# Kernel optimization log

Measured on AMD Instinct MI355X. Metric: run time of the kernel, lower is better.

Reference implementation:

```python
import jax, jax.numpy as jnp
import numpy as np

IC, IND, MID, OC, OD, ITERS = 8, 16, 32, 8, 16, 3
B, H, W = 8, 64, 64


def squash(x, axis):
    sq = jnp.sum(x * x, axis=axis, keepdims=True)
    return sq / (0.5 + sq) * x / (jnp.sqrt(sq + 1e-6) + 1e-6)


def gconv(x, w, b, pad):
    # grouped conv over the IC capsule groups (equivalent to the per-capsule
    # Conv2d blocks applied to slices of the capsule axis)
    y = jax.lax.conv_general_dilated(
        x, w, (1, 1), pad,
        dimension_numbers=("NCHW", "OIHW", "NCHW"),
        feature_group_count=IC)
    return y + b[None, :, None, None]


def setup_inputs() -> dict:
    key = jax.random.key(0)
    ks = jax.random.split(key, 7)
    x = jax.random.normal(ks[0], (B, IC * IND, H, W), jnp.float32)
    w1 = jax.random.normal(ks[1], (IC * MID, IND, 1, 1), jnp.float32) * 0.1
    b1 = jax.random.normal(ks[2], (IC * MID,), jnp.float32) * 0.1
    w2 = jax.random.normal(ks[3], (IC * MID, MID, 3, 3), jnp.float32) * 0.05
    b2 = jax.random.normal(ks[4], (IC * MID,), jnp.float32) * 0.1
    w3 = jax.random.normal(ks[5], (IC * OC * OD, MID, 1, 1), jnp.float32) * 0.05
    b3 = jax.random.normal(ks[6], (IC * OC * OD,), jnp.float32) * 0.1
    attn_w = jnp.zeros((1, OC, 1, 1, 1), jnp.float32)  # torch init: zeros
    attn_b = jnp.ones((1, OC, 1, 1, 1), jnp.float32)   # torch init: ones
    return dict(x=x, w1=w1, b1=b1, w2=w2, b2=b2, w3=w3, b3=b3,
                attn_w=attn_w, attn_b=attn_b)


def reference(x, w1, b1, w2, b2, w3, b3, attn_w, attn_b):
    bsz = x.shape[0]
    h_, w_ = x.shape[-2], x.shape[-1]
    # per-capsule conv stack: ReLU -> 1x1 -> ReLU -> 3x3 -> ReLU -> 1x1
    h = jax.nn.relu(x)
    h = jax.nn.relu(gconv(h, w1, b1, "VALID"))
    h = jax.nn.relu(gconv(h, w2, b2, "SAME"))
    h = gconv(h, w3, b3, "VALID")                     # [B, IC*OC*OD, H, W]
    u_hat = h.reshape(bsz, IC, OC, OD, h_, w_)
    u_sq = squash(u_hat, axis=3)
    # dynamic routing
    b = jnp.zeros((bsz, IC, OC, h_, w_), u_hat.dtype)
    for _ in range(ITERS - 1):
        c = jax.nn.sigmoid(b)
        s = jnp.sum(u_sq * c[:, :, :, None], axis=1)   # [B, OC, OD, H, W]
        v = squash(s, axis=2)
        b = b + jnp.sum(u_sq * v[:, None], axis=3)     # [B, IC, OC, H, W]
    c = jax.nn.sigmoid(b)
    s = jnp.sum(u_hat * c[:, :, :, None], axis=1)      # [B, OC, OD, H, W]
    # SpatialCapsuleAttn
    mean_hw = jnp.mean(s, axis=(-2, -1), keepdims=True)        # adaptive avg pool(1)
    avg = jnp.sum(s * mean_hw, axis=2)                         # [B, OC, H, W]
    t = avg.reshape(bsz, OC, h_ * w_)
    m = jnp.mean(t, axis=-1, keepdims=True)
    sd = jnp.std(t, axis=-1, keepdims=True, ddof=1) + 1e-6     # torch std: unbiased
    t = (t - m) / sd
    t = t.reshape(bsz, OC, 1, h_, w_) * attn_w + attn_b
    s = s * jax.nn.sigmoid(t)
    out = s.reshape(bsz, OC * OD, h_, w_) + x
    return out
```

## Files before the change

### kernel.cpp

```cpp
#include <hip/hip_runtime.h>
#include <hip/hip_bf16.h>
#include <hip/hip_fp16.h>

#define HW 4096

typedef _Float16 f16x8 __attribute__((ext_vector_type(8)));
typedef float f32x4 __attribute__((ext_vector_type(4)));

#define FOR8(X) X(0) X(1) X(2) X(3) X(4) X(5) X(6) X(7)

static __device__ __forceinline__ __half2 u2h(unsigned int u) {
    union { unsigned int u; __half2 h; } c; c.u = u; return c.h;
}
static __device__ __forceinline__ unsigned int h2u(__half2 h) {
    union { unsigned int u; __half2 h; } c; c.h = h; return c.u;
}

__global__ __launch_bounds__(256) void k0_prep(const float* __restrict__ w3, ushort* __restrict__ w3h,
                                               const float* __restrict__ w2, ushort* __restrict__ w2f) {
    int bid = blockIdx.x;
    int t = threadIdx.x;
    if (bid < 128) {
        int gi = bid * 256 + t;
        int j = gi & 7;
        int l = (gi >> 3) & 63;
        int p = gi >> 9;
        int ic = p >> 3, oc = p & 7;
        int od = l & 15;
        int m  = ((l >> 4) << 3) + j;
        w3h[gi] = __half_as_ushort(__float2half(w3[(size_t)((ic * 128 + oc * 16 + od) * 32 + m)]));
    } else {
        int gi = (bid - 128) * 256 + t;
        if (gi >= 73728) return;
        int j   = gi & 7;
        int l   = (gi >> 3) & 63;
        int h   = (gi >> 9) & 1;
        int tap = (gi >> 10) % 9;
        int g   = gi / 9216;
        int co = h * 16 + (l & 15);
        int ci = ((l >> 4) << 3) + j;
        w2f[gi] = __half_as_ushort(__float2half(w2[(size_t)((g * 32 + co) * 32 + ci) * 9 + tap]));
    }
}

__global__ __launch_bounds__(256) void k12_conv(const float* __restrict__ x, const float* __restrict__ w1,
                                                const float* __restrict__ b1, const ushort* __restrict__ w2f,
                                                const float* __restrict__ b2, ushort* __restrict__ h2g) {
    __shared__ ushort h1s[3][66][40];

    int bi = blockIdx.x;
    int y  = bi & 63;
    int g  = (bi >> 6) & 7;
    int b  = bi >> 9;
    int t  = threadIdx.x;

    if (t < 198) {
        int r  = t / 66;
        int xi = t - r * 66;
        int yy = y + r - 1;
        int xx = xi - 1;
        bool valid = (yy >= 0) && (yy < 64) && (xx >= 0) && (xx < 64);
        ushort hv[32];
        if (valid) {
            const float* xb = x + (size_t)(b * 128 + g * 16) * HW + yy * 64 + xx;
            float xv[16];
#pragma unroll
            for (int i = 0; i < 16; ++i) xv[i] = fmaxf(xb[i * HW], 0.f);
            const float* wg = w1 + g * 512;
            const float* bg = b1 + g * 32;
#pragma unroll
            for (int m = 0; m < 32; ++m) {
                float acc = bg[m];
#pragma unroll
                for (int i = 0; i < 16; ++i) acc = fmaf(xv[i], wg[m * 16 + i], acc);
                hv[m] = __half_as_ushort(__float2half(fmaxf(acc, 0.f)));
            }
        } else {
#pragma unroll
            for (int m = 0; m < 32; ++m) hv[m] = 0;
        }
        ushort* dst = &h1s[r][xi][0];
#pragma unroll
        for (int q = 0; q < 4; ++q) *(uint4*)&dst[q * 8] = *(uint4*)&hv[q * 8];
    }
    __syncthreads();

    int w  = t >> 6, l = t & 63;
    int lrow = l & 15, kgrp = l >> 4;
    int xcol = w * 16 + lrow;

    f16x8 Bf[9];
#pragma unroll
    for (int dy = 0; dy < 3; ++dy)
#pragma unroll
        for (int dx = 0; dx < 3; ++dx)
            Bf[dy * 3 + dx] = *(const f16x8*)&h1s[dy][xcol + dx][kgrp * 8];

    const ushort* wg2 = w2f + (size_t)g * 9216;
    f16x8 Af[9][2];
#pragma unroll
    for (int tap = 0; tap < 9; ++tap)
#pragma unroll
        for (int h = 0; h < 2; ++h)
            Af[tap][h] = *(const f16x8*)&wg2[((tap * 2 + h) * 64 + l) * 8];

    f32x4 acc[2];
#pragma unroll
    for (int h = 0; h < 2; ++h) {
        float4 bias = *(const float4*)(b2 + g * 32 + h * 16 + kgrp * 4);
        acc[h][0] = bias.x; acc[h][1] = bias.y; acc[h][2] = bias.z; acc[h][3] = bias.w;
    }
#pragma unroll
    for (int tap = 0; tap < 9; ++tap) {
#pragma unroll
        for (int h = 0; h < 2; ++h)
            acc[h] = __builtin_amdgcn_mfma_f32_16x16x32_f16(Af[tap][h], Bf[tap], acc[h], 0, 0, 0);
    }

    int px = y * 64 + xcol;
    ushort* ob = h2g + ((size_t)(b * 8 + g) * HW + px) * 32;
#pragma unroll
    for (int h = 0; h < 2; ++h) {
        __half2 lo = __floats2half2_rn(fmaxf(acc[h][0], 0.f), fmaxf(acc[h][1], 0.f));
        __half2 hi = __floats2half2_rn(fmaxf(acc[h][2], 0.f), fmaxf(acc[h][3], 0.f));
        uint2 wv; wv.x = h2u(lo); wv.y = h2u(hi);
        *(uint2*)&ob[h * 16 + kgrp * 4] = wv;
    }
}

__global__ __launch_bounds__(512) void k3f_route(const ushort* __restrict__ h2g, const ushort* __restrict__ w3h,
                                                 const float* __restrict__ b3, ushort* __restrict__ sOut,
                                                 float* __restrict__ part) {
    __shared__ ushort us[32 * 1024];
    __shared__ float wred[8][16][8];
    int bid = blockIdx.x;
    int b   = bid >> 7;
    int px0 = (bid & 127) << 5;
    int t   = threadIdx.x;
    int w   = t >> 6, l = t & 63;

    {
        int ic = w;
        int lrow = l & 15, lk = l >> 4;
        f16x8 bf0 = *(const f16x8*)&h2g[(((size_t)(b * 8 + ic)) * HW + px0 + lrow) * 32 + lk * 8];
        f16x8 bf1 = *(const f16x8*)&h2g[(((size_t)(b * 8 + ic)) * HW + px0 + 16 + lrow) * 32 + lk * 8];
        int s0sw = (lrow & 15) << 3;
#pragma unroll
        for (int oc = 0; oc < 8; ++oc) {
            f16x8 af = *(const f16x8*)&w3h[((ic * 8 + oc) * 64 + l) * 8];
            float4 bv = *(const float4*)(b3 + ic * 128 + oc * 16 + lk * 4);
            f32x4 c0; c0[0] = bv.x; c0[1] = bv.y; c0[2] = bv.z; c0[3] = bv.w;
            int ch = ic * 128 + oc * 16 + lk * 4;
            f32x4 d0 = __builtin_amdgcn_mfma_f32_16x16x32_f16(af, bf0, c0, 0, 0, 0);
            uint2 wv0;
            wv0.x = h2u(__floats2half2_rn(d0[0], d0[1]));
            wv0.y = h2u(__floats2half2_rn(d0[2], d0[3]));
            *(uint2*)&us[lrow * 1024 + (ch ^ s0sw)] = wv0;
            f32x4 d1 = __builtin_amdgcn_mfma_f32_16x16x32_f16(af, bf1, c0, 0, 0, 0);
            uint2 wv1;
            wv1.x = h2u(__floats2half2_rn(d1[0], d1[1]));
            wv1.y = h2u(__floats2half2_rn(d1[2], d1[3]));
            *(uint2*)&us[(16 + lrow) * 1024 + (ch ^ s0sw)] = wv1;
        }
    }
    __syncthreads();

    int px  = t >> 4;
    int oc  = (t >> 1) & 7;
    int odh = t & 1;
    int ssw = (px & 15) << 3;
    const ushort* ur = &us[px * 1024];
#define LDQ(i) uint4 q##i = *(const uint4*)&ur[((i) * 128 + oc * 16 + odh * 8) ^ ssw];
    FOR8(LDQ)
#undef LDQ
    __syncthreads();

#define UNP(i) float2 f0 = __half22float2(u2h(q##i.x)), f1 = __half22float2(u2h(q##i.y)), \
                      f2 = __half22float2(u2h(q##i.z)), f3 = __half22float2(u2h(q##i.w));

#define SC(i) float sc##i; { UNP(i) \
        float sp = f0.x*f0.x + f0.y*f0.y + f1.x*f1.x + f1.y*f1.y \
                 + f2.x*f2.x + f2.y*f2.y + f3.x*f3.x + f3.y*f3.y; \
        sp += __shfl_xor(sp, 1); \
        sc##i = sp / ((0.5f + sp) * (sqrtf(sp + 1e-6f) + 1e-6f)); }
    FOR8(SC)
#undef SC

#define BRI(i) float br##i = 0.f;
    FOR8(BRI)
#undef BRI

    float s0, s1, s2, s3, s4, s5, s6, s7;
#pragma unroll
    for (int it = 0; it < 2; ++it) {
#define CSC(i) float cs##i = sc##i / (1.f + __expf(-br##i));
        FOR8(CSC)
#undef CSC
        s0 = s1 = s2 = s3 = s4 = s5 = s6 = s7 = 0.f;
#define SVA(i) { UNP(i) \
        s0 = fmaf(f0.x, cs##i, s0); s1 = fmaf(f0.y, cs##i, s1); \
        s2 = fmaf(f1.x, cs##i, s2); s3 = fmaf(f1.y, cs##i, s3); \
        s4 = fmaf(f2.x, cs##i, s4); s5 = fmaf(f2.y, cs##i, s5); \
        s6 = fmaf(f3.x, cs##i, s6); s7 = fmaf(f3.y, cs##i, s7); }
        FOR8(SVA)
#undef SVA
        float sp = s0*s0 + s1*s1 + s2*s2 + s3*s3 + s4*s4 + s5*s5 + s6*s6 + s7*s7;
        sp += __shfl_xor(sp, 1);
        float f = sp / ((0.5f + sp) * (sqrtf(sp + 1e-6f) + 1e-6f));
#define DOTD(i) { UNP(i) \
        float dp = f0.x*s0 + f0.y*s1 + f1.x*s2 + f1.y*s3 + f2.x*s4 + f2.y*s5 + f3.x*s6 + f3.y*s7; \
        dp += __shfl_xor(dp, 1); \
        br##i = fmaf(sc##i * f, dp, br##i); }
        FOR8(DOTD)
#undef DOTD
    }

#define CF(i) float cf##i = 1.f / (1.f + __expf(-br##i));
    FOR8(CF)
#undef CF
    s0 = s1 = s2 = s3 = s4 = s5 = s6 = s7 = 0.f;
#define FS(i) { UNP(i) \
        s0 = fmaf(f0.x, cf##i, s0); s1 = fmaf(f0.y, cf##i, s1); \
        s2 = fmaf(f1.x, cf##i, s2); s3 = fmaf(f1.y, cf##i, s3); \
        s4 = fmaf(f2.x, cf##i, s4); s5 = fmaf(f2.y, cf##i, s5); \
        s6 = fmaf(f3.x, cf##i, s6); s7 = fmaf(f3.y, cf##i, s7); }
    FOR8(FS)
#undef FS
#undef UNP

    {
        uint4 pk;
        pk.x = h2u(__floats2half2_rn(s0, s1));
        pk.y = h2u(__floats2half2_rn(s2, s3));
        pk.z = h2u(__floats2half2_rn(s4, s5));
        pk.w = h2u(__floats2half2_rn(s6, s7));
        *(uint4*)&us[px * 1024 + ((oc * 16 + odh * 8) ^ ssw)] = pk;
    }

    {
        float p0 = s0, p1 = s1, p2 = s2, p3 = s3, p4 = s4, p5 = s5, p6 = s6, p7 = s7;
#pragma unroll
        for (int m = 16; m <= 32; m <<= 1) {
            p0 += __shfl_xor(p0, m); p1 += __shfl_xor(p1, m);
            p2 += __shfl_xor(p2, m); p3 += __shfl_xor(p3, m);
            p4 += __shfl_xor(p4, m); p5 += __shfl_xor(p5, m);
            p6 += __shfl_xor(p6, m); p7 += __shfl_xor(p7, m);
        }
        if ((l & 48) == 0) {
            float* wr = wred[w][oc * 2 + odh];
            wr[0] = p0; wr[1] = p1; wr[2] = p2; wr[3] = p3;
            wr[4] = p4; wr[5] = p5; wr[6] = p6; wr[7] = p7;
        }
    }
    __syncthreads();

    {
        int oc2 = w;
        int pxw = l >> 1, half = l & 1;
        int ch2 = (oc2 * 16 + half * 8) ^ ((pxw & 15) << 3);
        uint4 v = *(const uint4*)&us[pxw * 1024 + ch2];
        ushort* sb = sOut + ((size_t)(b * 8 + oc2) * 4096 + px0 + pxw) * 16 + half * 8;
        *(uint4*)sb = v;
    }
    if (t < 128) {
        int comb = t >> 3, j = t & 7;
        float a = 0.f;
#pragma unroll
        for (int ww = 0; ww < 8; ++ww) a += wred[ww][comb][j];
        int oc3 = comb >> 1, odh3 = comb & 1;
        part[((size_t)(b * 8 + oc3) * 128 + (bid & 127)) * 16 + odh3 * 8 + j] = a;
    }
}

__global__ __launch_bounds__(256) void k4_avg(const ushort* __restrict__ sIn, const float* __restrict__ part,
                                              float* __restrict__ avg, float* __restrict__ stats) {
    __shared__ float mh[16];
    int bi = blockIdx.x;
    int chunk = bi & 15;
    int bo = bi >> 4;
    int t = threadIdx.x;
    int pos = chunk * 256 + t;

    if (t < 16) {
        float a = 0.f;
        for (int c = 0; c < 128; ++c) a += part[(size_t)(bo * 128 + c) * 16 + t];
        mh[t] = a * (1.f / 4096.f);
    }
    __syncthreads();

    const ushort* sb = sIn + ((size_t)bo * 4096 + pos) * 16;
    uint4 qa = *(const uint4*)&sb[0];
    uint4 qb = *(const uint4*)&sb[8];
    float2 f0 = __half22float2(u2h(qa.x)), f1 = __half22float2(u2h(qa.y));
    float2 f2 = __half22float2(u2h(qa.z)), f3 = __half22float2(u2h(qa.w));
    float2 f4 = __half22float2(u2h(qb.x)), f5 = __half22float2(u2h(qb.y));
    float2 f6 = __half22float2(u2h(qb.z)), f7 = __half22float2(u2h(qb.w));
    float a = f0.x * mh[0] + f0.y * mh[1] + f1.x * mh[2] + f1.y * mh[3]
            + f2.x * mh[4] + f2.y * mh[5] + f3.x * mh[6] + f3.y * mh[7]
            + f4.x * mh[8] + f4.y * mh[9] + f5.x * mh[10] + f5.y * mh[11]
            + f6.x * mh[12] + f6.y * mh[13] + f7.x * mh[14] + f7.y * mh[15];
    avg[(size_t)bo * 4096 + pos] = a;

    float p1 = a, p2 = a * a;
#pragma unroll
    for (int m = 1; m < 64; m <<= 1) {
        p1 += __shfl_xor(p1, m);
        p2 += __shfl_xor(p2, m);
    }
    if ((t & 63) == 0) {
        atomicAdd(&stats[bo * 2],     p1);
        atomicAdd(&stats[bo * 2 + 1], p2);
    }
}

__global__ __launch_bounds__(256) void k5_out(const ushort* __restrict__ sIn, const float* __restrict__ x,
                                              const float* __restrict__ avg, const float* __restrict__ stats,
                                              const float* __restrict__ aw, const float* __restrict__ ab,
                                              float* __restrict__ out) {
    int bi = blockIdx.x;
    int chunk = bi & 15;
    int bo = bi >> 4;
    int oc = bo & 7;
    int pos = chunk * 256 + threadIdx.x;

    float sum = stats[bo * 2], sumsq = stats[bo * 2 + 1];
    float m   = sum * (1.f / 4096.f);
    float var = (sumsq - 4096.f * m * m) * (1.f / 4095.f);
    float sd  = sqrtf(fmaxf(var, 0.f)) + 1e-6f;

    float t   = (avg[(size_t)bo * 4096 + pos] - m) / sd * aw[oc] + ab[oc];
    float sig = 1.f / (1.f + __expf(-t));

    const ushort* sb = sIn + ((size_t)bo * 4096 + pos) * 16;
    uint4 qa = *(const uint4*)&sb[0];
    uint4 qb = *(const uint4*)&sb[8];
    float2 f0 = __half22float2(u2h(qa.x)), f1 = __half22float2(u2h(qa.y));
    float2 f2 = __half22float2(u2h(qa.z)), f3 = __half22float2(u2h(qa.w));
    float2 f4 = __half22float2(u2h(qb.x)), f5 = __half22float2(u2h(qb.y));
    float2 f6 = __half22float2(u2h(qb.z)), f7 = __half22float2(u2h(qb.w));
    float sv[16] = {f0.x, f0.y, f1.x, f1.y, f2.x, f2.y, f3.x, f3.y,
                    f4.x, f4.y, f5.x, f5.y, f6.x, f6.y, f7.x, f7.y};

    const float* xb = x + (size_t)bo * 16 * HW + pos;
    float* ob = out + (size_t)bo * 16 * HW + pos;
#pragma unroll
    for (int od = 0; od < 16; ++od) ob[od * HW] = fmaf(sv[od], sig, xb[od * HW]);
}

extern "C" void kernel_launch(void* const* d_in, const int* in_sizes, int n_in,
                              void* d_out, int out_size, void* d_ws, size_t ws_size,
                              hipStream_t stream) {
    const float* x  = (const float*)d_in[0];
    const float* w1 = (const float*)d_in[1];
    const float* b1 = (const float*)d_in[2];
    const float* w2 = (const float*)d_in[3];
    const float* b2 = (const float*)d_in[4];
    const float* w3 = (const float*)d_in[5];
    const float* b3 = (const float*)d_in[6];
    const float* aw = (const float*)d_in[7];
    const float* ab = (const float*)d_in[8];

    float* ws      = (float*)d_ws;
    ushort* h2g    = (ushort*)ws;
    ushort* sbuf   = (ushort*)(ws + 4194304);
    float* avg     = ws + 4194304 + 2097152;
    float* part    = avg + 262144;
    float* stats   = part + 131072;
    ushort* w3h    = (ushort*)(stats + 128);
    ushort* w2f    = w3h + 32768;

    hipMemsetAsync(stats, 0, 128 * sizeof(float), stream);
    k0_prep  <<<416, 256, 0, stream>>>(w3, w3h, w2, w2f);
    k12_conv <<<4096, 256, 0, stream>>>(x, w1, b1, w2f, b2, h2g);
    k3f_route<<<1024, 512, 0, stream>>>(h2g, w3h, b3, sbuf, part);
    k4_avg   <<<1024, 256, 0, stream>>>(sbuf, part, avg, stats);
    k5_out   <<<1024, 256, 0, stream>>>(sbuf, x, avg, stats, aw, ab, (float*)d_out);
}
```

Before: 94.33 us.

## Process four output rows per conv block to reuse halo rows; fold stats memset into prep

The fused 1x1+3x3 conv kernel now computes four output rows per block instead of one. It stages six input rows of the 1x1 output in shared memory rather than three, so halo recomputation drops from 3x to 1.5x, and the grid shrinks fourfold. Each wave loops over four 16-column tiles and loads its A and B fragments per tap inside the loop instead of preloading them. The separate hipMemsetAsync for the stats buffer is replaced by zeroing it in the prep kernel, which removes one launch. The trade-offs are fewer blocks in flight, lower parallelism, and repeated weight loads from global or L1 memory inside the tile loop.

```diff
diff --git a/kernel.cpp b/kernel.cpp
--- a/kernel.cpp
+++ b/kernel.cpp
@@ -17,9 +17,11 @@
 }
 
 __global__ __launch_bounds__(256) void k0_prep(const float* __restrict__ w3, ushort* __restrict__ w3h,
-                                               const float* __restrict__ w2, ushort* __restrict__ w2f) {
+                                               const float* __restrict__ w2, ushort* __restrict__ w2f,
+                                               float* __restrict__ stats) {
     int bid = blockIdx.x;
     int t = threadIdx.x;
+    if (bid == 0 && t < 128) stats[t] = 0.f;
     if (bid < 128) {
         int gi = bid * 256 + t;
         int j = gi & 7;
@@ -46,18 +48,19 @@
 __global__ __launch_bounds__(256) void k12_conv(const float* __restrict__ x, const float* __restrict__ w1,
                                                 const float* __restrict__ b1, const ushort* __restrict__ w2f,
                                                 const float* __restrict__ b2, ushort* __restrict__ h2g) {
-    __shared__ ushort h1s[3][66][40];
+    __shared__ ushort h1s[6][66][40];
 
     int bi = blockIdx.x;
-    int y  = bi & 63;
-    int g  = (bi >> 6) & 7;
-    int b  = bi >> 9;
+    int q  = bi & 15;
+    int g  = (bi >> 4) & 7;
+    int b  = bi >> 7;
+    int y0 = q * 4;
     int t  = threadIdx.x;
 
-    if (t < 198) {
-        int r  = t / 66;
-        int xi = t - r * 66;
-        int yy = y + r - 1;
+    for (int i = t; i < 396; i += 256) {
+        int r  = i / 66;
+        int xi = i - r * 66;
+        int yy = y0 + r - 1;
         int xx = xi - 1;
         bool valid = (yy >= 0) && (yy < 64) && (xx >= 0) && (xx < 64);
         ushort hv[32];
@@ -65,14 +68,14 @@
             const float* xb = x + (size_t)(b * 128 + g * 16) * HW + yy * 64 + xx;
             float xv[16];
 #pragma unroll
-            for (int i = 0; i < 16; ++i) xv[i] = fmaxf(xb[i * HW], 0.f);
+            for (int i2 = 0; i2 < 16; ++i2) xv[i2] = fmaxf(xb[i2 * HW], 0.f);
             const float* wg = w1 + g * 512;
             const float* bg = b1 + g * 32;
 #pragma unroll
             for (int m = 0; m < 32; ++m) {
                 float acc = bg[m];
 #pragma unroll
-                for (int i = 0; i < 16; ++i) acc = fmaf(xv[i], wg[m * 16 + i], acc);
+                for (int i2 = 0; i2 < 16; ++i2) acc = fmaf(xv[i2], wg[m * 16 + i2], acc);
                 hv[m] = __half_as_ushort(__float2half(fmaxf(acc, 0.f)));
             }
         } else {
@@ -81,50 +84,42 @@
         }
         ushort* dst = &h1s[r][xi][0];
 #pragma unroll
-        for (int q = 0; q < 4; ++q) *(uint4*)&dst[q * 8] = *(uint4*)&hv[q * 8];
+        for (int q2 = 0; q2 < 4; ++q2) *(uint4*)&dst[q2 * 8] = *(uint4*)&hv[q2 * 8];
     }
     __syncthreads();
 
     int w  = t >> 6, l = t & 63;
     int lrow = l & 15, kgrp = l >> 4;
-    int xcol = w * 16 + lrow;
-
-    f16x8 Bf[9];
-#pragma unroll
-    for (int dy = 0; dy < 3; ++dy)
-#pragma unroll
-        for (int dx = 0; dx < 3; ++dx)
-            Bf[dy * 3 + dx] = *(const f16x8*)&h1s[dy][xcol + dx][kgrp * 8];
-
+    int yloc = w;
     const ushort* wg2 = w2f + (size_t)g * 9216;
-    f16x8 Af[9][2];
-#pragma unroll
-    for (int tap = 0; tap < 9; ++tap)
-#pragma unroll
-        for (int h = 0; h < 2; ++h)
-            Af[tap][h] = *(const f16x8*)&wg2[((tap * 2 + h) * 64 + l) * 8];
-
-    f32x4 acc[2];
-#pragma unroll
-    for (int h = 0; h < 2; ++h) {
-        float4 bias = *(const float4*)(b2 + g * 32 + h * 16 + kgrp * 4);
-        acc[h][0] = bias.x; acc[h][1] = bias.y; acc[h][2] = bias.z; acc[h][3] = bias.w;
-    }
-#pragma unroll
-    for (int tap = 0; tap < 9; ++tap) {
-#pragma unroll
-        for (int h = 0; h < 2; ++h)
-            acc[h] = __builtin_amdgcn_mfma_f32_16x16x32_f16(Af[tap][h], Bf[tap], acc[h], 0, 0, 0);
-    }
-
-    int px = y * 64 + xcol;
-    ushort* ob = h2g + ((size_t)(b * 8 + g) * HW + px) * 32;
-#pragma unroll
-    for (int h = 0; h < 2; ++h) {
-        __half2 lo = __floats2half2_rn(fmaxf(acc[h][0], 0.f), fmaxf(acc[h][1], 0.f));
-        __half2 hi = __floats2half2_rn(fmaxf(acc[h][2], 0.f), fmaxf(acc[h][3], 0.f));
-        uint2 wv; wv.x = h2u(lo); wv.y = h2u(hi);
-        *(uint2*)&ob[h * 16 + kgrp * 4] = wv;
+
+    float4 bias0 = *(const float4*)(b2 + g * 32 + kgrp * 4);
+    float4 bias1 = *(const float4*)(b2 + g * 32 + 16 + kgrp * 4);
+
+#pragma unroll
+    for (int tile = 0; tile < 4; ++tile) {
+        int xcol = tile * 16 + lrow;
+        f32x4 acc0, acc1;
+        acc0[0] = bias0.x; acc0[1] = bias0.y; acc0[2] = bias0.z; acc0[3] = bias0.w;
+        acc1[0] = bias1.x; acc1[1] = bias1.y; acc1[2] = bias1.z; acc1[3] = bias1.w;
+#pragma unroll
+        for (int tap = 0; tap < 9; ++tap) {
+            int dy = tap / 3, dx = tap - dy * 3;
+            f16x8 Bf = *(const f16x8*)&h1s[yloc + dy][xcol + dx][kgrp * 8];
+            f16x8 A0 = *(const f16x8*)&wg2[((tap * 2 + 0) * 64 + l) * 8];
+            f16x8 A1 = *(const f16x8*)&wg2[((tap * 2 + 1) * 64 + l) * 8];
+            acc0 = __builtin_amdgcn_mfma_f32_16x16x32_f16(A0, Bf, acc0, 0, 0, 0);
+            acc1 = __builtin_amdgcn_mfma_f32_16x16x32_f16(A1, Bf, acc1, 0, 0, 0);
+        }
+        int px = (y0 + yloc) * 64 + xcol;
+        ushort* ob = h2g + ((size_t)(b * 8 + g) * HW + px) * 32;
+        uint2 wv0, wv1;
+        wv0.x = h2u(__floats2half2_rn(fmaxf(acc0[0], 0.f), fmaxf(acc0[1], 0.f)));
+        wv0.y = h2u(__floats2half2_rn(fmaxf(acc0[2], 0.f), fmaxf(acc0[3], 0.f)));
+        wv1.x = h2u(__floats2half2_rn(fmaxf(acc1[0], 0.f), fmaxf(acc1[1], 0.f)));
+        wv1.y = h2u(__floats2half2_rn(fmaxf(acc1[2], 0.f), fmaxf(acc1[3], 0.f)));
+        *(uint2*)&ob[kgrp * 4] = wv0;
+        *(uint2*)&ob[16 + kgrp * 4] = wv1;
     }
 }
 
@@ -369,9 +364,8 @@
     ushort* w3h    = (ushort*)(stats + 128);
     ushort* w2f    = w3h + 32768;
 
-    hipMemsetAsync(stats, 0, 128 * sizeof(float), stream);
-    k0_prep  <<<416, 256, 0, stream>>>(w3, w3h, w2, w2f);
-    k12_conv <<<4096, 256, 0, stream>>>(x, w1, b1, w2f, b2, h2g);
+    k0_prep  <<<416, 256, 0, stream>>>(w3, w3h, w2, w2f, stats);
+    k12_conv <<<1024, 256, 0, stream>>>(x, w1, b1, w2f, b2, h2g);
     k3f_route<<<1024, 512, 0, stream>>>(h2g, w3h, b3, sbuf, part);
     k4_avg   <<<1024, 256, 0, stream>>>(sbuf, part, avg, stats);
     k5_out   <<<1024, 256, 0, stream>>>(sbuf, x, avg, stats, aw, ab, (float*)d_out);
```

Measured after the change: 85.63 us. -9.2%, faster.
